# Kernel tuning notes

Hardware: AMD Instinct MI355X
Metric: run time of the kernel (lower is better)

Reference implementation:

```python
import jax, jax.numpy as jnp
import numpy as np

L = 16384          # leaves of complete binary tree
D = 256            # word_dim == tree_input_dim == output_dim
V = 50257          # num_words
NL = 5             # num_labels


def setup_inputs() -> dict:
    key = jax.random.key(0)
    ks = jax.random.split(key, 8)
    s = 0.05
    return {
        "tokens": jax.random.randint(ks[0], (L,), 0, V),
        "emb": jax.random.normal(ks[1], (V, D), jnp.float32) * s,      # word_embedding.weight
        "Wx": jax.random.normal(ks[2], (D, 5 * D), jnp.float32) * s,   # input->gates (leaf only)
        "Ul": jax.random.normal(ks[3], (D, 5 * D), jnp.float32) * s,   # left-child h -> gates
        "Ur": jax.random.normal(ks[4], (D, 5 * D), jnp.float32) * s,   # right-child h -> gates
        "b": jnp.zeros((5 * D,), jnp.float32),
        "Wp": jax.random.normal(ks[5], (D, NL), jnp.float32) * s,      # pred_layer
        "bp": jnp.zeros((NL,), jnp.float32),
    }


def _cell(pre, c_l, c_r):
    # Binary TreeLSTM cell: gates [i, f_l, f_r, o, u]
    i, fl, fr, o, u = jnp.split(pre, 5, axis=-1)
    c = jax.nn.sigmoid(i) * jnp.tanh(u) + jax.nn.sigmoid(fl) * c_l + jax.nn.sigmoid(fr) * c_r
    h = jax.nn.sigmoid(o) * jnp.tanh(c)
    return h, c


def reference(tokens, emb, Wx, Ul, Ur, b, Wp, bp):
    # dropout layers are identity at inference (no-op here)
    x = emb[tokens]                                  # [L, D] seq_output == word embeddings (leaf_rnn=False)
    # leaf nodes: l/r child states are zeros, inputs = seq_out[idx]
    h, c = _cell(x @ Wx + b, 0.0, 0.0)               # [L, D]
    hs = [h]
    # internal nodes level by level (complete binary tree): inputs=None -> no Wx term
    while h.shape[0] > 1:
        hl, hr = h[0::2], h[1::2]
        cl, cr = c[0::2], c[1::2]
        h, c = _cell(hl @ Ul + hr @ Ur + b, cl, cr)
        hs.append(h)
    hidden = jnp.concatenate(hs, axis=0)             # [2L-1, D] all node hidden states
    return hidden @ Wp + bp                          # single_h_pred logits [2L-1, NL]
```

## Files before the change

kernel.cpp:

```cpp
#include <hip/hip_runtime.h>
#include <hip/hip_bf16.h>
#include <math.h>
#include <stdint.h>


typedef __attribute__((ext_vector_type(8))) short     bf16x8;
typedef __attribute__((ext_vector_type(4))) float     f32x4;
typedef __attribute__((ext_vector_type(8))) unsigned short u16x8;

#define NGATE 5
#define TAIL_T0 3

__device__ __forceinline__ uint16_t f2bf(float f) {
    uint32_t u = __builtin_bit_cast(uint32_t, f);
    u = (u + 0x7fffu + ((u >> 16) & 1u)) >> 16;
    return (uint16_t)u;
}
__device__ __forceinline__ float bf2f(uint16_t h) {
    uint32_t u = ((uint32_t)h) << 16;
    return __builtin_bit_cast(float, u);
}
__device__ __forceinline__ float sigf(float x) { return 1.0f / (1.0f + __expf(-x)); }
__device__ __forceinline__ float tanhfast(float x) {
    float e = __expf(2.0f * x);
    return (e - 1.0f) / (e + 1.0f);
}

__device__ __forceinline__ void gld_lds16(const void* g, void* l) {
    __builtin_amdgcn_global_load_lds(
        (const __attribute__((address_space(1))) void*)g,
        (__attribute__((address_space(3))) void*)l,
        16, 0, 0);
}

__global__ __launch_bounds__(256) void pack_w_kernel(
    const float* __restrict__ W0, const float* __restrict__ W1, int KT,
    uint16_t* __restrict__ dhi, uint16_t* __restrict__ dlo)
{
    int gid = blockIdx.x * 256 + threadIdx.x;
    int total = 80 * KT * 64;
    if (gid >= total) return;
    int lane = gid & 63;
    int n  = ((gid >> 6) / KT) * 16 + (lane & 15);
    int kt = (gid >> 6) % KT;
    int k0 = kt * 32 + (lane >> 4) * 8;
    u16x8 vh, vl;
    #pragma unroll
    for (int j = 0; j < 8; ++j) {
        int k = k0 + j;
        const float* src = (k < 256) ? (W0 + (size_t)k * 1280)
                                     : (W1 + (size_t)(k - 256) * 1280);
        float v = src[n];
        uint16_t h = f2bf(v);
        vh[j] = h;
        vl[j] = f2bf(v - bf2f(h));
    }
    *(u16x8*)(dhi + (size_t)gid * 8) = vh;
    *(u16x8*)(dlo + (size_t)gid * 8) = vl;
}

template<int BM, int KT, int JT, bool LVL0>
__global__ __launch_bounds__(256) void lvl_gemm(
    const uint16_t* __restrict__ Ahi, const uint16_t* __restrict__ Alo,
    const int* __restrict__ tokens, const float* __restrict__ emb,
    const uint16_t* __restrict__ Bhi, const uint16_t* __restrict__ Blo,
    const float* __restrict__ b,
    const float* __restrict__ c_prev,
    uint16_t* __restrict__ h_hi_out, uint16_t* __restrict__ h_lo_out,
    float* __restrict__ c_out, int n)
{
    constexpr int K   = KT * 32;
    constexpr int MT  = BM / 64;
    constexpr int NC  = NGATE * JT * 2;

    __shared__ __align__(16) uint16_t sB0[NC * 512];
    __shared__ __align__(16) uint16_t sB1[NC * 512];

    const int tid  = threadIdx.x;
    const int wave = tid >> 6;
    const int lane = tid & 63;
    const int quad = lane >> 4;
    const int l15  = lane & 15;
    const int r0   = blockIdx.x * BM;
    const int jn   = blockIdx.y;

    f32x4 acc[MT][JT][NGATE] = {};

    const uint16_t* aph[MT];
    const uint16_t* apl[MT];
    const float*    ebase[MT];
    #pragma unroll
    for (int mt = 0; mt < MT; ++mt) {
        int row = r0 + (wave * MT + mt) * 16 + l15;
        row = min(row, n - 1);
        if constexpr (LVL0) {
            int tok = tokens[row];
            ebase[mt] = emb + (size_t)tok * 256 + quad * 8;
        } else {
            aph[mt] = Ahi + (size_t)row * K + quad * 8;
            apl[mt] = Alo + (size_t)row * K + quad * 8;
        }
    }

    auto stageB = [&](uint16_t* dB, int kt) {
        for (int c = wave; c < NC; c += 4) {
            int hl = c & 1, gj = c >> 1;
            const uint16_t* src = hl ? Blo : Bhi;
            int nt = (gj / JT) * 16 + jn * JT + (gj % JT);
            gld_lds16(src + ((size_t)(nt * KT + kt) * 64 + lane) * 8,
                      dB + c * 512);
        }
    };
    auto loadAn = [&](bf16x8 (&ah)[MT], bf16x8 (&al)[MT], int kt) {
        #pragma unroll
        for (int mt = 0; mt < MT; ++mt) {
            ah[mt] = *(const bf16x8*)(aph[mt] + kt * 32);
            al[mt] = *(const bf16x8*)(apl[mt] + kt * 32);
        }
    };
    auto loadA0 = [&](float4 (&e)[MT][2], int kt) {
        #pragma unroll
        for (int mt = 0; mt < MT; ++mt) {
            const float4* p = (const float4*)(ebase[mt] + kt * 32);
            e[mt][0] = p[0];
            e[mt][1] = p[1];
        }
    };
    auto cvtA0 = [&](const float4 (&e)[MT][2], bf16x8 (&ah)[MT], bf16x8 (&al)[MT]) {
        #pragma unroll
        for (int mt = 0; mt < MT; ++mt) {
            float fv[8];
            fv[0] = e[mt][0].x; fv[1] = e[mt][0].y; fv[2] = e[mt][0].z; fv[3] = e[mt][0].w;
            fv[4] = e[mt][1].x; fv[5] = e[mt][1].y; fv[6] = e[mt][1].z; fv[7] = e[mt][1].w;
            #pragma unroll
            for (int j = 0; j < 8; ++j) {
                uint16_t h = f2bf(fv[j]);
                ah[mt][j] = (short)h;
                al[mt][j] = (short)f2bf(fv[j] - bf2f(h));
            }
        }
    };
    auto mfma_all = [&](const bf16x8 (&ah)[MT], const bf16x8 (&al)[MT],
                        const uint16_t* Bx) {
        #pragma unroll
        for (int g = 0; g < NGATE; ++g) {
            #pragma unroll
            for (int js = 0; js < JT; ++js) {
                const uint16_t* bp = Bx + (g * JT + js) * 1024;
                bf16x8 bh = *(const bf16x8*)(bp + lane * 8);
                bf16x8 bl = *(const bf16x8*)(bp + 512 + lane * 8);
                #pragma unroll
                for (int mt = 0; mt < MT; ++mt) {
                    acc[mt][js][g] = __builtin_amdgcn_mfma_f32_16x16x32_bf16(ah[mt], bh, acc[mt][js][g], 0, 0, 0);
                    acc[mt][js][g] = __builtin_amdgcn_mfma_f32_16x16x32_bf16(al[mt], bh, acc[mt][js][g], 0, 0, 0);
                    acc[mt][js][g] = __builtin_amdgcn_mfma_f32_16x16x32_bf16(ah[mt], bl, acc[mt][js][g], 0, 0, 0);
                }
            }
        }
    };

    if constexpr (LVL0) {
        float4 eA[MT][2], eB[MT][2];
        loadA0(eA, 0);
        stageB(sB0, 0);
        __syncthreads();
        for (int kt = 0; kt < KT; kt += 2) {
            loadA0(eB, kt + 1);
            stageB(sB1, kt + 1);
            {
                bf16x8 ah[MT], al[MT];
                cvtA0(eA, ah, al);
                mfma_all(ah, al, sB0);
            }
            __syncthreads();
            if (kt + 2 < KT) { loadA0(eA, kt + 2); stageB(sB0, kt + 2); }
            {
                bf16x8 ah[MT], al[MT];
                cvtA0(eB, ah, al);
                mfma_all(ah, al, sB1);
            }
            __syncthreads();
        }
    } else {
        bf16x8 hA[MT], lA[MT], hB[MT], lB[MT];
        loadAn(hA, lA, 0);
        stageB(sB0, 0);
        __syncthreads();
        for (int kt = 0; kt < KT; kt += 2) {
            loadAn(hB, lB, kt + 1);
            stageB(sB1, kt + 1);
            mfma_all(hA, lA, sB0);
            __syncthreads();
            if (kt + 2 < KT) { loadAn(hA, lA, kt + 2); stageB(sB0, kt + 2); }
            mfma_all(hB, lB, sB1);
            __syncthreads();
        }
    }

    const int d0 = (jn * JT) * 16 + l15;
    float bg[JT][NGATE];
    #pragma unroll
    for (int js = 0; js < JT; ++js)
        #pragma unroll
        for (int g = 0; g < NGATE; ++g) bg[js][g] = b[g * 256 + d0 + js * 16];

    #pragma unroll
    for (int mt = 0; mt < MT; ++mt) {
        int rb = r0 + wave * (MT * 16) + mt * 16 + quad * 4;
        #pragma unroll
        for (int v = 0; v < 4; ++v) {
            int row = rb + v;
            if (row < n) {
                #pragma unroll
                for (int js = 0; js < JT; ++js) {
                    int d = d0 + js * 16;
                    float gi = acc[mt][js][0][v] + bg[js][0];
                    float fl = acc[mt][js][1][v] + bg[js][1];
                    float fr = acc[mt][js][2][v] + bg[js][2];
                    float go = acc[mt][js][3][v] + bg[js][3];
                    float gu = acc[mt][js][4][v] + bg[js][4];
                    float cc;
                    if constexpr (LVL0) {
                        cc = sigf(gi) * tanhfast(gu);
                        (void)fl; (void)fr;
                    } else {
                        float cl = c_prev[(size_t)(2 * row) * 256 + d];
                        float cr = c_prev[(size_t)(2 * row + 1) * 256 + d];
                        cc = sigf(gi) * tanhfast(gu) + sigf(fl) * cl + sigf(fr) * cr;
                    }
                    float hh = sigf(go) * tanhfast(cc);
                    uint16_t hb = f2bf(hh);
                    h_hi_out[(size_t)row * 256 + d] = hb;
                    h_lo_out[(size_t)row * 256 + d] = f2bf(hh - bf2f(hb));
                    c_out[(size_t)row * 256 + d] = cc;
                }
            }
        }
    }
}

struct TailFrags {
    bf16x8 a0h, a0l, a1h, a1l;
    bf16x8 b0h, b1h, b2h, b3h, b4h;
    bf16x8 b0l, b1l, b2l, b3l, b4l;
};

#define TL_LOAD(F, KTG) do {                                                  \
    F.a0h = *(const bf16x8*)(a0hp + (KTG) * 32);                              \
    F.a0l = *(const bf16x8*)(a0lp + (KTG) * 32);                              \
    F.a1h = *(const bf16x8*)(a1hp + (KTG) * 32);                              \
    F.a1l = *(const bf16x8*)(a1lp + (KTG) * 32);                              \
    F.b0h = *(const bf16x8*)(bHp + 0 * 131072 + (KTG) * 512);                 \
    F.b1h = *(const bf16x8*)(bHp + 1 * 131072 + (KTG) * 512);                 \
    F.b2h = *(const bf16x8*)(bHp + 2 * 131072 + (KTG) * 512);                 \
    F.b3h = *(const bf16x8*)(bHp + 3 * 131072 + (KTG) * 512);                 \
    F.b4h = *(const bf16x8*)(bHp + 4 * 131072 + (KTG) * 512);                 \
    F.b0l = *(const bf16x8*)(bLp + 0 * 131072 + (KTG) * 512);                 \
    F.b1l = *(const bf16x8*)(bLp + 1 * 131072 + (KTG) * 512);                 \
    F.b2l = *(const bf16x8*)(bLp + 2 * 131072 + (KTG) * 512);                 \
    F.b3l = *(const bf16x8*)(bLp + 3 * 131072 + (KTG) * 512);                 \
    F.b4l = *(const bf16x8*)(bLp + 4 * 131072 + (KTG) * 512);                 \
} while (0)

#define TL_MM3(ACC, AH, AL, BH, BL2)                                          \
    ACC = __builtin_amdgcn_mfma_f32_16x16x32_bf16(AH, BH, ACC, 0, 0, 0);      \
    ACC = __builtin_amdgcn_mfma_f32_16x16x32_bf16(AL, BH, ACC, 0, 0, 0);      \
    ACC = __builtin_amdgcn_mfma_f32_16x16x32_bf16(AH, BL2, ACC, 0, 0, 0);

#define TL_STEP(F) do {                                                       \
    TL_MM3(acc00, F.a0h, F.a0l, F.b0h, F.b0l)                                 \
    TL_MM3(acc01, F.a0h, F.a0l, F.b1h, F.b1l)                                 \
    TL_MM3(acc02, F.a0h, F.a0l, F.b2h, F.b2l)                                 \
    TL_MM3(acc03, F.a0h, F.a0l, F.b3h, F.b3l)                                 \
    TL_MM3(acc04, F.a0h, F.a0l, F.b4h, F.b4l)                                 \
    TL_MM3(acc10, F.a1h, F.a1l, F.b0h, F.b0l)                                 \
    TL_MM3(acc11, F.a1h, F.a1l, F.b1h, F.b1l)                                 \
    TL_MM3(acc12, F.a1h, F.a1l, F.b2h, F.b2l)                                 \
    TL_MM3(acc13, F.a1h, F.a1l, F.b3h, F.b3l)                                 \
    TL_MM3(acc14, F.a1h, F.a1l, F.b4h, F.b4l)                                 \
} while (0)

#define TL_RST(M, G, A) {                                                     \
    r[(M)*20 + (G)*4 + 0] = A[0]; r[(M)*20 + (G)*4 + 1] = A[1];               \
    r[(M)*20 + (G)*4 + 2] = A[2]; r[(M)*20 + (G)*4 + 3] = A[3]; }

#define TL_RADD(M, G, A) {                                                    \
    A[0] += r[(M)*20 + (G)*4 + 0]; A[1] += r[(M)*20 + (G)*4 + 1];             \
    A[2] += r[(M)*20 + (G)*4 + 2]; A[3] += r[(M)*20 + (G)*4 + 3]; }

#define TL_EPI(M, A0, A1, A2, A3, A4) do {                                    \
    int rb = (mt0 + (M)) * 16 + quad * 4;                                     \
    _Pragma("unroll")                                                         \
    for (int v = 0; v < 4; ++v) {                                             \
        int row = rb + v;                                                     \
        if (row < n) {                                                        \
            float gi = A0[v] + bias[0 * 256 + d];                             \
            float fl = A1[v] + bias[1 * 256 + d];                             \
            float fr = A2[v] + bias[2 * 256 + d];                             \
            float go = A3[v] + bias[3 * 256 + d];                             \
            float gu = A4[v] + bias[4 * 256 + d];                             \
            float cl = c_in[(size_t)(2 * row) * 256 + d];                     \
            float cr = c_in[(size_t)(2 * row + 1) * 256 + d];                 \
            float cc = sigf(gi) * tanhfast(gu) + sigf(fl) * cl + sigf(fr) * cr; \
            float hhv = sigf(go) * tanhfast(cc);                              \
            uint16_t hb = f2bf(hhv);                                          \
            hh_out[(size_t)row * 256 + d] = hb;                               \
            hl_out[(size_t)row * 256 + d] = f2bf(hhv - bf2f(hb));             \
            c_out[(size_t)row * 256 + d] = cc;                                \
        }                                                                     \
    }                                                                         \
} while (0)

__global__ __launch_bounds__(256) void tail_lvl(
    const uint16_t* __restrict__ Ah, const uint16_t* __restrict__ Al,
    const uint16_t* __restrict__ BuH, const uint16_t* __restrict__ BuL,
    const float* __restrict__ bias, const float* __restrict__ c_in,
    uint16_t* __restrict__ hh_out, uint16_t* __restrict__ hl_out,
    float* __restrict__ c_out, int n)
{
    __shared__ float red[3][64][41];

    const int tid  = threadIdx.x;
    const int wave = tid >> 6;
    const int lane = tid & 63;
    const int quad = lane >> 4;
    const int l15  = lane & 15;
    const int mt0  = blockIdx.x * 2;
    const int jn   = blockIdx.y;

    int row0 = mt0 * 16 + l15;        if (row0 > n - 1) row0 = n - 1;
    int row1 = (mt0 + 1) * 16 + l15;  if (row1 > n - 1) row1 = n - 1;
    const uint16_t* a0hp = Ah + (size_t)row0 * 512 + quad * 8;
    const uint16_t* a0lp = Al + (size_t)row0 * 512 + quad * 8;
    const uint16_t* a1hp = Ah + (size_t)row1 * 512 + quad * 8;
    const uint16_t* a1lp = Al + (size_t)row1 * 512 + quad * 8;
    const uint16_t* bHp  = BuH + (size_t)jn * 8192 + lane * 8;
    const uint16_t* bLp  = BuL + (size_t)jn * 8192 + lane * 8;
    const int kb = wave * 4;

    f32x4 acc00 = {}, acc01 = {}, acc02 = {}, acc03 = {}, acc04 = {};
    f32x4 acc10 = {}, acc11 = {}, acc12 = {}, acc13 = {}, acc14 = {};

    TailFrags f0, f1;
    TL_LOAD(f0, kb + 0);
    TL_LOAD(f1, kb + 1);
    TL_STEP(f0);
    TL_LOAD(f0, kb + 2);
    TL_STEP(f1);
    TL_LOAD(f1, kb + 3);
    TL_STEP(f0);
    TL_STEP(f1);

    if (wave != 0) {
        float* r = &red[wave - 1][lane][0];
        TL_RST(0, 0, acc00) TL_RST(0, 1, acc01) TL_RST(0, 2, acc02)
        TL_RST(0, 3, acc03) TL_RST(0, 4, acc04)
        TL_RST(1, 0, acc10) TL_RST(1, 1, acc11) TL_RST(1, 2, acc12)
        TL_RST(1, 3, acc13) TL_RST(1, 4, acc14)
    }
    __syncthreads();
    if (wave == 0) {
        #pragma unroll
        for (int k = 0; k < 3; ++k) {
            const float* r = &red[k][lane][0];
            TL_RADD(0, 0, acc00) TL_RADD(0, 1, acc01) TL_RADD(0, 2, acc02)
            TL_RADD(0, 3, acc03) TL_RADD(0, 4, acc04)
            TL_RADD(1, 0, acc10) TL_RADD(1, 1, acc11) TL_RADD(1, 2, acc12)
            TL_RADD(1, 3, acc13) TL_RADD(1, 4, acc14)
        }
        const int d = jn * 16 + l15;
        TL_EPI(0, acc00, acc01, acc02, acc03, acc04);
        TL_EPI(1, acc10, acc11, acc12, acc13, acc14);
    }
}

__global__ __launch_bounds__(256) void proj_kernel(
    const uint16_t* __restrict__ h_hi, const uint16_t* __restrict__ h_lo,
    const float* __restrict__ Wp, const float* __restrict__ bp,
    float* __restrict__ out, int n)
{
    const int wave = blockIdx.x * 4 + (threadIdx.x >> 6);
    const int lane = threadIdx.x & 63;
    if (wave >= n) return;

    const uint16_t* hh = h_hi + (size_t)wave * 256;
    const uint16_t* hl = h_lo + (size_t)wave * 256;
    float s[5] = {0.f, 0.f, 0.f, 0.f, 0.f};
    #pragma unroll
    for (int q = 0; q < 4; ++q) {
        int dd = lane + 64 * q;
        float hv = bf2f(hh[dd]) + bf2f(hl[dd]);
        #pragma unroll
        for (int j = 0; j < 5; ++j) s[j] += hv * Wp[dd * 5 + j];
    }
    #pragma unroll
    for (int off = 32; off; off >>= 1)
        #pragma unroll
        for (int j = 0; j < 5; ++j) s[j] += __shfl_down(s[j], off);

    if (lane == 0) {
        #pragma unroll
        for (int j = 0; j < 5; ++j) out[(size_t)wave * 5 + j] = s[j] + bp[j];
    }
}

extern "C" void kernel_launch(void* const* d_in, const int* in_sizes, int n_in,
                              void* d_out, int out_size, void* d_ws, size_t ws_size,
                              hipStream_t stream)
{
    const int*   tokens = (const int*)  d_in[0];
    const float* emb    = (const float*)d_in[1];
    const float* Wx     = (const float*)d_in[2];
    const float* Ul     = (const float*)d_in[3];
    const float* Ur     = (const float*)d_in[4];
    const float* b      = (const float*)d_in[5];
    const float* Wp     = (const float*)d_in[6];
    const float* bp     = (const float*)d_in[7];
    float* out = (float*)d_out;

    uint8_t* w = (uint8_t*)d_ws;
    uint16_t* h_hi = (uint16_t*)w;  w += (size_t)32767 * 256 * 2;
    uint16_t* h_lo = (uint16_t*)w;  w += (size_t)32767 * 256 * 2;
    float*    cA   = (float*)w;     w += (size_t)16384 * 256 * 4;
    float*    cB   = (float*)w;     w += (size_t)8192  * 256 * 4;
    uint16_t* BxH  = (uint16_t*)w;  w += (size_t)80 * 8  * 64 * 8 * 2;
    uint16_t* BxL  = (uint16_t*)w;  w += (size_t)80 * 8  * 64 * 8 * 2;
    uint16_t* BuH  = (uint16_t*)w;  w += (size_t)80 * 16 * 64 * 8 * 2;
    uint16_t* BuL  = (uint16_t*)w;  w += (size_t)80 * 16 * 64 * 8 * 2;

    pack_w_kernel<<<(80 * 8  * 64) / 256, 256, 0, stream>>>(Wx, Wx, 8,  BxH, BxL);
    pack_w_kernel<<<(80 * 16 * 64) / 256, 256, 0, stream>>>(Ul, Ur, 16, BuH, BuL);

    int off[16];
    off[0] = 0;
    for (int t = 0; t < 15; ++t) off[t + 1] = off[t] + (16384 >> t);

    lvl_gemm<128, 8, 2, true><<<dim3(16384 / 128, 8), 256, 0, stream>>>(
        nullptr, nullptr, tokens, emb, BxH, BxL, b, nullptr,
        h_hi, h_lo, cA, 16384);

    for (int t = 1; t < TAIL_T0; ++t) {
        int n = 16384 >> t;
        const uint16_t* Ahp = h_hi + (size_t)off[t - 1] * 256;
        const uint16_t* Alp = h_lo + (size_t)off[t - 1] * 256;
        float* c_in  = (t % 2 == 0) ? cB : cA;
        float* c_out = (t % 2 == 0) ? cA : cB;
        uint16_t* Hh = h_hi + (size_t)off[t] * 256;
        uint16_t* Hl = h_lo + (size_t)off[t] * 256;
        lvl_gemm<128, 16, 2, false><<<dim3(n / 128, 8), 256, 0, stream>>>(
            Ahp, Alp, nullptr, nullptr, BuH, BuL, b, c_in, Hh, Hl, c_out, n);
    }

    for (int t = TAIL_T0; t <= 14; ++t) {
        int n = 16384 >> t;
        const uint16_t* Ahp = h_hi + (size_t)off[t - 1] * 256;
        const uint16_t* Alp = h_lo + (size_t)off[t - 1] * 256;
        float* c_in  = (t % 2 == 0) ? cB : cA;
        float* c_out = (t % 2 == 0) ? cA : cB;
        uint16_t* Hh = h_hi + (size_t)off[t] * 256;
        uint16_t* Hl = h_lo + (size_t)off[t] * 256;
        int mtiles = (n + 15) >> 4;
        int gx = (mtiles + 1) >> 1;
        tail_lvl<<<dim3(gx, 16), 256, 0, stream>>>(
            Ahp, Alp, BuH, BuL, b, c_in, Hh, Hl, c_out, n);
    }

    int total = off[15];
    proj_kernel<<<(total + 3) / 4, 256, 0, stream>>>(h_hi, h_lo, Wp, bp, out, total);
}
```

Before: 331.6 us.

## Merge tail tree levels into one cooperative persistent kernel with grid barrier

Tree levels from 5 upward run inside a single cooperative kernel of 16 blocks, one per 16-column slice. Each block loops over the row tiles of a level, and levels are separated by an atomic-counter grid barrier. This is meant to remove the per-level kernel launch overhead for small levels. In exchange, the early merged levels lose parallelism because they are processed serially by only 16 blocks. If the cooperative launch fails, the code falls back to per-level launches.

```diff
diff --git a/kernel.cpp b/kernel.cpp
--- a/kernel.cpp
+++ b/kernel.cpp
@@ -10,6 +10,7 @@
 
 #define NGATE 5
 #define TAIL_T0 3
+#define MERGE_T0 5
 
 __device__ __forceinline__ uint16_t f2bf(float f) {
     uint32_t u = __builtin_bit_cast(uint32_t, f);
@@ -311,6 +312,40 @@
     }                                                                         \
 } while (0)
 
+#define TL_BODY do {                                                          \
+    f32x4 acc00 = {}, acc01 = {}, acc02 = {}, acc03 = {}, acc04 = {};         \
+    f32x4 acc10 = {}, acc11 = {}, acc12 = {}, acc13 = {}, acc14 = {};         \
+    TailFrags f0, f1;                                                         \
+    TL_LOAD(f0, kb + 0);                                                      \
+    TL_LOAD(f1, kb + 1);                                                      \
+    TL_STEP(f0);                                                              \
+    TL_LOAD(f0, kb + 2);                                                      \
+    TL_STEP(f1);                                                              \
+    TL_LOAD(f1, kb + 3);                                                      \
+    TL_STEP(f0);                                                              \
+    TL_STEP(f1);                                                              \
+    if (wave != 0) {                                                          \
+        float* r = &red[wave - 1][lane][0];                                   \
+        TL_RST(0, 0, acc00) TL_RST(0, 1, acc01) TL_RST(0, 2, acc02)           \
+        TL_RST(0, 3, acc03) TL_RST(0, 4, acc04)                               \
+        TL_RST(1, 0, acc10) TL_RST(1, 1, acc11) TL_RST(1, 2, acc12)           \
+        TL_RST(1, 3, acc13) TL_RST(1, 4, acc14)                               \
+    }                                                                         \
+    __syncthreads();                                                          \
+    if (wave == 0) {                                                          \
+        _Pragma("unroll")                                                     \
+        for (int k = 0; k < 3; ++k) {                                         \
+            const float* r = &red[k][lane][0];                                \
+            TL_RADD(0, 0, acc00) TL_RADD(0, 1, acc01) TL_RADD(0, 2, acc02)    \
+            TL_RADD(0, 3, acc03) TL_RADD(0, 4, acc04)                         \
+            TL_RADD(1, 0, acc10) TL_RADD(1, 1, acc11) TL_RADD(1, 2, acc12)    \
+            TL_RADD(1, 3, acc13) TL_RADD(1, 4, acc14)                         \
+        }                                                                     \
+        TL_EPI(0, acc00, acc01, acc02, acc03, acc04);                         \
+        TL_EPI(1, acc10, acc11, acc12, acc13, acc14);                         \
+    }                                                                         \
+} while (0)
+
 __global__ __launch_bounds__(256) void tail_lvl(
     const uint16_t* __restrict__ Ah, const uint16_t* __restrict__ Al,
     const uint16_t* __restrict__ BuH, const uint16_t* __restrict__ BuL,
@@ -337,40 +372,70 @@
     const uint16_t* bHp  = BuH + (size_t)jn * 8192 + lane * 8;
     const uint16_t* bLp  = BuL + (size_t)jn * 8192 + lane * 8;
     const int kb = wave * 4;
-
-    f32x4 acc00 = {}, acc01 = {}, acc02 = {}, acc03 = {}, acc04 = {};
-    f32x4 acc10 = {}, acc11 = {}, acc12 = {}, acc13 = {}, acc14 = {};
-
-    TailFrags f0, f1;
-    TL_LOAD(f0, kb + 0);
-    TL_LOAD(f1, kb + 1);
-    TL_STEP(f0);
-    TL_LOAD(f0, kb + 2);
-    TL_STEP(f1);
-    TL_LOAD(f1, kb + 3);
-    TL_STEP(f0);
-    TL_STEP(f1);
-
-    if (wave != 0) {
-        float* r = &red[wave - 1][lane][0];
-        TL_RST(0, 0, acc00) TL_RST(0, 1, acc01) TL_RST(0, 2, acc02)
-        TL_RST(0, 3, acc03) TL_RST(0, 4, acc04)
-        TL_RST(1, 0, acc10) TL_RST(1, 1, acc11) TL_RST(1, 2, acc12)
-        TL_RST(1, 3, acc13) TL_RST(1, 4, acc14)
-    }
-    __syncthreads();
-    if (wave == 0) {
-        #pragma unroll
-        for (int k = 0; k < 3; ++k) {
-            const float* r = &red[k][lane][0];
-            TL_RADD(0, 0, acc00) TL_RADD(0, 1, acc01) TL_RADD(0, 2, acc02)
-            TL_RADD(0, 3, acc03) TL_RADD(0, 4, acc04)
-            TL_RADD(1, 0, acc10) TL_RADD(1, 1, acc11) TL_RADD(1, 2, acc12)
-            TL_RADD(1, 3, acc13) TL_RADD(1, 4, acc14)
-        }
-        const int d = jn * 16 + l15;
-        TL_EPI(0, acc00, acc01, acc02, acc03, acc04);
-        TL_EPI(1, acc10, acc11, acc12, acc13, acc14);
+    const int d  = jn * 16 + l15;
+
+    TL_BODY;
+}
+
+__global__ __launch_bounds__(256) void tail_merged(
+    uint16_t* h_hi, uint16_t* h_lo,
+    const uint16_t* __restrict__ BuH, const uint16_t* __restrict__ BuL,
+    const float* __restrict__ bias,
+    float* cA, float* cB,
+    unsigned int* sync_cnt, int t0)
+{
+    __shared__ float red[3][64][41];
+
+    const int tid  = threadIdx.x;
+    const int wave = tid >> 6;
+    const int lane = tid & 63;
+    const int quad = lane >> 4;
+    const int l15  = lane & 15;
+    const int jn   = blockIdx.x;
+
+    const uint16_t* bHp = BuH + (size_t)jn * 8192 + lane * 8;
+    const uint16_t* bLp = BuL + (size_t)jn * 8192 + lane * 8;
+    const int kb = wave * 4;
+    const int d  = jn * 16 + l15;
+
+    for (int t = t0; t <= 14; ++t) {
+        const int n = 16384 >> t;
+        const size_t offp = 32768u - (32768u >> (t - 1));
+        const size_t offc = 32768u - (32768u >> t);
+        const uint16_t* Ah = h_hi + offp * 256;
+        const uint16_t* Al = h_lo + offp * 256;
+        const float* c_in  = (t & 1) ? cA : cB;
+        float*       c_out = (t & 1) ? cB : cA;
+        uint16_t* hh_out = h_hi + offc * 256;
+        uint16_t* hl_out = h_lo + offc * 256;
+        const int mtiles = (n + 15) >> 4;
+        const int mpairs = (mtiles + 1) >> 1;
+
+        for (int mp = 0; mp < mpairs; ++mp) {
+            const int mt0 = mp * 2;
+            int row0 = mt0 * 16 + l15;        if (row0 > n - 1) row0 = n - 1;
+            int row1 = (mt0 + 1) * 16 + l15;  if (row1 > n - 1) row1 = n - 1;
+            const uint16_t* a0hp = Ah + (size_t)row0 * 512 + quad * 8;
+            const uint16_t* a0lp = Al + (size_t)row0 * 512 + quad * 8;
+            const uint16_t* a1hp = Ah + (size_t)row1 * 512 + quad * 8;
+            const uint16_t* a1lp = Al + (size_t)row1 * 512 + quad * 8;
+
+            TL_BODY;
+            __syncthreads();
+        }
+
+        if (t < 14) {
+            __threadfence();
+            __syncthreads();
+            if (tid == 0) {
+                unsigned int tgt = 16u * (unsigned int)(t - t0 + 1);
+                atomicAdd(sync_cnt, 1u);
+                while (atomicAdd(sync_cnt, 0u) < tgt)
+                    __builtin_amdgcn_s_sleep(16);
+            }
+            __syncthreads();
+            __threadfence();
+        }
     }
 }
 
@@ -427,6 +492,7 @@
     uint16_t* BxL  = (uint16_t*)w;  w += (size_t)80 * 8  * 64 * 8 * 2;
     uint16_t* BuH  = (uint16_t*)w;  w += (size_t)80 * 16 * 64 * 8 * 2;
     uint16_t* BuL  = (uint16_t*)w;  w += (size_t)80 * 16 * 64 * 8 * 2;
+    unsigned int* sync_cnt = (unsigned int*)w;  w += 128;
 
     pack_w_kernel<<<(80 * 8  * 64) / 256, 256, 0, stream>>>(Wx, Wx, 8,  BxH, BxL);
     pack_w_kernel<<<(80 * 16 * 64) / 256, 256, 0, stream>>>(Ul, Ur, 16, BuH, BuL);
@@ -451,7 +517,7 @@
             Ahp, Alp, nullptr, nullptr, BuH, BuL, b, c_in, Hh, Hl, c_out, n);
     }
 
-    for (int t = TAIL_T0; t <= 14; ++t) {
+    for (int t = TAIL_T0; t < MERGE_T0; ++t) {
         int n = 16384 >> t;
         const uint16_t* Ahp = h_hi + (size_t)off[t - 1] * 256;
         const uint16_t* Alp = h_lo + (size_t)off[t - 1] * 256;
@@ -465,6 +531,32 @@
             Ahp, Alp, BuH, BuL, b, c_in, Hh, Hl, c_out, n);
     }
 
+    {
+        hipMemsetAsync(sync_cnt, 0, sizeof(unsigned int), stream);
+        int t0 = MERGE_T0;
+        void* targs[] = { (void*)&h_hi, (void*)&h_lo, (void*)&BuH, (void*)&BuL,
+                          (void*)&b, (void*)&cA, (void*)&cB,
+                          (void*)&sync_cnt, (void*)&t0 };
+        hipError_t e = hipLaunchCooperativeKernel(
+            (const void*)tail_merged, dim3(16), dim3(256), targs, 0, stream);
+        if (e != hipSuccess) {
+            (void)hipGetLastError();
+            for (int t = MERGE_T0; t <= 14; ++t) {
+                int n = 16384 >> t;
+                const uint16_t* Ahp = h_hi + (size_t)off[t - 1] * 256;
+                const uint16_t* Alp = h_lo + (size_t)off[t - 1] * 256;
+                float* c_in  = (t % 2 == 0) ? cB : cA;
+                float* c_out = (t % 2 == 0) ? cA : cB;
+                uint16_t* Hh = h_hi + (size_t)off[t] * 256;
+                uint16_t* Hl = h_lo + (size_t)off[t] * 256;
+                int mtiles = (n + 15) >> 4;
+                int gx = (mtiles + 1) >> 1;
+                tail_lvl<<<dim3(gx, 16), 256, 0, stream>>>(
+                    Ahp, Alp, BuH, BuL, b, c_in, Hh, Hl, c_out, n);
+            }
+        }
+    }
+
     int total = off[15];
     proj_kernel<<<(total + 3) / 4, 256, 0, stream>>>(h_hi, h_lo, Wp, bp, out, total);
 }
```

New measurement: 630.6 us. 90.2% more time.
